# Performance work log

Measured on AMD Instinct MI355X. Metric: run time of the kernel, lower is better.

The kernel has to match this reference:

```python
import jax, jax.numpy as jnp
import numpy as np

NUM_USERS = 100000
NUM_ITEMS = 50000
EMBED_DIM = 64
N_LAYERS = 3
NUM_EDGES = 3276800  # avg user degree 32
BATCH = 16384


def setup_inputs() -> dict:
    key = jax.random.key(0)
    k0, k1, k2, k3, k4, k5 = jax.random.split(key, 6)
    rows = jax.random.randint(k0, (NUM_EDGES,), 0, NUM_USERS, dtype=jnp.int32)
    cols = jax.random.randint(k1, (NUM_EDGES,), 0, NUM_ITEMS, dtype=jnp.int32)
    user_table = jax.random.normal(k2, (NUM_USERS, EMBED_DIM), dtype=jnp.float32) * 0.1
    item_table = jax.random.normal(k3, (NUM_ITEMS, EMBED_DIM), dtype=jnp.float32) * 0.1
    user_indices = jax.random.randint(k4, (BATCH,), 0, NUM_USERS, dtype=jnp.int32)
    item_indices = jax.random.randint(k5, (BATCH,), 0, NUM_ITEMS, dtype=jnp.int32)
    return {
        "user_table": user_table,
        "item_table": item_table,
        "rows": rows,
        "cols": cols,
        "user_indices": user_indices,
        "item_indices": item_indices,
    }


def reference(user_table, item_table, rows, cols, user_indices, item_indices):
    # D^-1 A row-normalization of the binary bipartite adjacency:
    # normalized edge value for edge (u, i) is 1 / deg(u) (0 if isolated).
    ones = jnp.ones(rows.shape, dtype=user_table.dtype)
    deg = jax.ops.segment_sum(ones, rows, num_segments=NUM_USERS)
    inv_deg = jnp.where(deg > 0, 1.0 / deg, 0.0)
    vals = inv_deg[rows]  # [E]

    u = user_table  # [U, D] (unused by propagation in the original too)
    it = item_table  # [I, D]
    for _ in range(N_LAYERS):
        # u = A @ it  (SpMM via gather + segment-sum over destination users)
        u = jax.ops.segment_sum(vals[:, None] * it[cols], rows, num_segments=NUM_USERS)
        # it = A^T @ u
        it = jax.ops.segment_sum(vals[:, None] * u[rows], cols, num_segments=NUM_ITEMS)

    scores = jnp.sum(u[user_indices] * it[item_indices], axis=-1)  # [B]
    return jax.nn.sigmoid(scores)
```

## Files before the change

### kernel.cpp

```cpp
#include <hip/hip_runtime.h>
#include <math.h>

#define NUM_USERS 100000
#define NUM_ITEMS 50000
#define EMBED     64
#define NUM_EDGES 3276800
#define BATCH     16384
#define CAP       12800
#define NBUCK     391
#define P1_EDGES  8192
#define P1_THREADS 512
#define P2_THREADS 1024
#define CVT_GROUPS (NUM_ITEMS * 8)
#define CVT_BLOCKS ((CVT_GROUPS + P1_THREADS - 1) / P1_THREADS)

typedef _Float16 half8 __attribute__((ext_vector_type(8)));

__global__ void __launch_bounds__(P1_THREADS)
build_kernel(const int* __restrict__ rows, const int* __restrict__ cols,
             const float* __restrict__ itab, _Float16* __restrict__ it16,
             _Float16* __restrict__ w16,
             int* __restrict__ ucur, int* __restrict__ icur,
             int* __restrict__ rec_u, int* __restrict__ rec_i) {
    __shared__ int hu[400], hi[400], gu[400], gi[400];
    __shared__ int lbase[400], lcur[400];
    __shared__ int sc[512];
    __shared__ int recbuf[P1_EDGES];
    int t = threadIdx.x;

    if (blockIdx.x >= 400) {
        int b = blockIdx.x - 400;
        if (b < CVT_BLOCKS) {
            int i = b * P1_THREADS + t;
            if (i < CVT_GROUPS) {
                const float4* p = (const float4*)itab + 2 * i;
                float4 a = p[0], c = p[1];
                half8 o;
                o[0] = (_Float16)a.x; o[1] = (_Float16)a.y; o[2] = (_Float16)a.z; o[3] = (_Float16)a.w;
                o[4] = (_Float16)c.x; o[5] = (_Float16)c.y; o[6] = (_Float16)c.z; o[7] = (_Float16)c.w;
                ((half8*)it16)[i] = o;
            }
        } else {
            if (t < 64) w16[(long long)NUM_USERS * EMBED + t] = (_Float16)0.f;
            else if (t < 128) it16[(long long)NUM_ITEMS * EMBED + (t - 64)] = (_Float16)0.f;
        }
        return;
    }

    long long e0 = (long long)blockIdx.x * P1_EDGES;
    int er[16], ec[16];
    #pragma unroll
    for (int q = 0; q < 16; ++q) {
        er[q] = rows[e0 + t + q * P1_THREADS];
        ec[q] = cols[e0 + t + q * P1_THREADS];
    }

    for (int i = t; i < 400; i += P1_THREADS) { hu[i] = 0; hi[i] = 0; }
    __syncthreads();
    #pragma unroll
    for (int q = 0; q < 16; ++q) {
        atomicAdd(&hu[er[q] >> 8], 1);
        atomicAdd(&hi[ec[q] >> 7], 1);
    }
    __syncthreads();
    for (int i = t; i < 400; i += P1_THREADS) {
        int vr = (hu[i] + 15) & ~15;
        gu[i] = vr ? atomicAdd(&ucur[i], vr) : 0;
        vr = (hi[i] + 15) & ~15;
        gi[i] = vr ? atomicAdd(&icur[i], vr) : 0;
    }

    __syncthreads();
    sc[t] = (t < 400) ? hu[t] : 0;
    __syncthreads();
    for (int o = 1; o < 512; o <<= 1) {
        int x = (t >= o) ? sc[t - o] : 0; __syncthreads();
        sc[t] += x; __syncthreads();
    }
    if (t < 400) { lbase[t] = sc[t] - hu[t]; lcur[t] = 0; }
    __syncthreads();
    #pragma unroll
    for (int q = 0; q < 16; ++q) {
        int b = er[q] >> 8;
        int p = lbase[b] + atomicAdd(&lcur[b], 1);
        recbuf[p] = (ec[q] << 8) | (er[q] & 255);
    }
    __syncthreads();
    sc[t] = (t < 400) ? ((hu[t] + 15) & ~15) : 0;
    __syncthreads();
    for (int o = 1; o < 512; o <<= 1) {
        int x = (t >= o) ? sc[t - o] : 0; __syncthreads();
        sc[t] += x; __syncthreads();
    }
    int total = sc[511];
    for (int o4 = t * 4; o4 < total; o4 += P1_THREADS * 4) {
        int lo = 0, hi_ = 399;
        while (lo < hi_) { int mid = (lo + hi_) >> 1; if (sc[mid] > o4) hi_ = mid; else lo = mid + 1; }
        int b = lo;
        int v = hu[b];
        int vr = (v + 15) & ~15;
        int j = o4 - (sc[b] - vr);
        int gpos = gu[b] + j;
        if (gpos + 3 < CAP) {
            int4 val;
            val.x = (j + 0 < v) ? recbuf[lbase[b] + j + 0] : -1;
            val.y = (j + 1 < v) ? recbuf[lbase[b] + j + 1] : -1;
            val.z = (j + 2 < v) ? recbuf[lbase[b] + j + 2] : -1;
            val.w = (j + 3 < v) ? recbuf[lbase[b] + j + 3] : -1;
            *(int4*)(rec_u + (long long)b * CAP + gpos) = val;
        } else {
            for (int k = 0; k < 4; ++k)
                if (gpos + k < CAP)
                    rec_u[(long long)b * CAP + gpos + k] = (j + k < v) ? recbuf[lbase[b] + j + k] : -1;
        }
    }

    __syncthreads();
    sc[t] = (t < 400) ? hi[t] : 0;
    __syncthreads();
    for (int o = 1; o < 512; o <<= 1) {
        int x = (t >= o) ? sc[t - o] : 0; __syncthreads();
        sc[t] += x; __syncthreads();
    }
    if (t < 400) { lbase[t] = sc[t] - hi[t]; lcur[t] = 0; }
    __syncthreads();
    #pragma unroll
    for (int q = 0; q < 16; ++q) {
        int b = ec[q] >> 7;
        int p = lbase[b] + atomicAdd(&lcur[b], 1);
        recbuf[p] = (er[q] << 7) | (ec[q] & 127);
    }
    __syncthreads();
    sc[t] = (t < 400) ? ((hi[t] + 15) & ~15) : 0;
    __syncthreads();
    for (int o = 1; o < 512; o <<= 1) {
        int x = (t >= o) ? sc[t - o] : 0; __syncthreads();
        sc[t] += x; __syncthreads();
    }
    total = sc[511];
    for (int o4 = t * 4; o4 < total; o4 += P1_THREADS * 4) {
        int lo = 0, hi_ = 399;
        while (lo < hi_) { int mid = (lo + hi_) >> 1; if (sc[mid] > o4) hi_ = mid; else lo = mid + 1; }
        int b = lo;
        int v = hi[b];
        int vr = (v + 15) & ~15;
        int j = o4 - (sc[b] - vr);
        int gpos = gi[b] + j;
        if (gpos + 3 < CAP) {
            int4 val;
            val.x = (j + 0 < v) ? recbuf[lbase[b] + j + 0] : -1;
            val.y = (j + 1 < v) ? recbuf[lbase[b] + j + 1] : -1;
            val.z = (j + 2 < v) ? recbuf[lbase[b] + j + 2] : -1;
            val.w = (j + 3 < v) ? recbuf[lbase[b] + j + 3] : -1;
            *(int4*)(rec_i + (long long)b * CAP + gpos) = val;
        } else {
            for (int k = 0; k < 4; ++k)
                if (gpos + k < CAP)
                    rec_i[(long long)b * CAP + gpos + k] = (j + k < v) ? recbuf[lbase[b] + j + k] : -1;
        }
    }
}

template <int VBITS>
__device__ __forceinline__ void pass2_body(int* __restrict__ rec, const int* __restrict__ cur,
                                           int* __restrict__ deg, int* __restrict__ off,
                                           float* __restrict__ inv32, int ncap, int b,
                                           int* buf, int* h, int* ex, int* cnt, int* sc) {
    const int V = 1 << VBITS, M = V - 1;
    int t = threadIdx.x;
    long long s = (long long)b * CAP;
    int n = cur[b]; if (n > CAP) n = CAP;
    int nv = (n + 3) >> 2;
    const int4* rec4 = (const int4*)(rec + s);
    for (int i = t; i < nv; i += P2_THREADS) {
        int4 v4 = rec4[i];
        buf[4 * i + 0] = v4.x; buf[4 * i + 1] = v4.y;
        buf[4 * i + 2] = v4.z; buf[4 * i + 3] = v4.w;
    }
    if (t < V) { h[t] = 0; cnt[t] = 0; }
    __syncthreads();
    for (int i = t; i < n; i += P2_THREADS) {
        int r = buf[i];
        if (r != -1) atomicAdd(&h[r & M], 1);
    }
    __syncthreads();
    if (t < V) sc[t] = h[t];
    __syncthreads();
    for (int o = 1; o < V; o <<= 1) {
        int x = (t >= o && t < V) ? sc[t - o] : 0;
        __syncthreads();
        if (t < V) sc[t] += x;
        __syncthreads();
    }
    if (t < V) {
        ex[t] = sc[t] - h[t];
        int id = b * V + t;
        if (id < ncap) {
            int v = h[t];
            deg[id] = v;
            off[id] = (int)(s + ex[t]);
            if (inv32) inv32[id] = v ? 1.0f / (float)v : 0.0f;
        }
    }
    __syncthreads();
    for (int i = t; i < n; i += P2_THREADS) {
        int r = buf[i];
        if (r == -1) continue;
        int k = r & M;
        int rnk = atomicAdd(&cnt[k], 1);
        rec[s + ex[k] + rnk] = (int)(((unsigned)r) >> VBITS);
    }
}

__global__ void __launch_bounds__(P2_THREADS)
pass2_kernel(int* __restrict__ rec_u, const int* __restrict__ ucur,
             int* __restrict__ udeg, int* __restrict__ uoff, float* __restrict__ inv32,
             int* __restrict__ rec_i, const int* __restrict__ icur,
             int* __restrict__ ideg, int* __restrict__ ioff) {
    __shared__ int buf[CAP];
    __shared__ int h[256], ex[256], cnt[256], sc[256];
    if (blockIdx.x < NBUCK)
        pass2_body<8>(rec_u, ucur, udeg, uoff, inv32, NUM_USERS, blockIdx.x,
                      buf, h, ex, cnt, sc);
    else
        pass2_body<7>(rec_i, icur, ideg, ioff, (float*)nullptr, NUM_ITEMS,
                      blockIdx.x - NBUCK, buf, h, ex, cnt, sc);
}

__global__ void gather_u(const int* __restrict__ uoff, const int* __restrict__ udeg,
                         const int* __restrict__ csr_col, const float* __restrict__ inv32,
                         const _Float16* __restrict__ it, _Float16* __restrict__ w) {
    int row = blockIdx.x * 4 + (threadIdx.x >> 6);
    if (row >= NUM_USERS) return;
    int lane = threadIdx.x & 63;
    int slot = lane >> 3;
    int h    = lane & 7;
    int start = uoff[row];
    int end = start + udeg[row];
    half8 acc = {0, 0, 0, 0, 0, 0, 0, 0};
    for (int k = start; k < end; k += 64) {
        int e1 = end - 1;
        int idx[8], c[8];
        #pragma unroll
        for (int q = 0; q < 8; ++q) {
            idx[q] = k + slot + q * 8;
            int safe = idx[q] < e1 ? idx[q] : e1;
            c[q] = csr_col[safe];
            c[q] = idx[q] < end ? c[q] : NUM_ITEMS;
        }
        half8 x[8];
        #pragma unroll
        for (int q = 0; q < 8; ++q)
            x[q] = *(const half8*)(it + (long long)c[q] * EMBED + (h << 3));
        #pragma unroll
        for (int q = 0; q < 8; ++q) acc += x[q];
    }
    float f[8];
    #pragma unroll
    for (int j = 0; j < 8; ++j) {
        f[j] = (float)acc[j];
        f[j] += __shfl_xor(f[j], 8, 64);
        f[j] += __shfl_xor(f[j], 16, 64);
        f[j] += __shfl_xor(f[j], 32, 64);
    }
    if (lane < 8) {
        float v = inv32[row];
        float v2 = v * v;
        half8 ow;
        #pragma unroll
        for (int j = 0; j < 8; ++j) ow[j] = (_Float16)(f[j] * v2);
        *(half8*)(w + (long long)row * EMBED + (lane << 3)) = ow;
    }
}

__global__ void gather_it(const int* __restrict__ ioff, const int* __restrict__ ideg,
                          const int* __restrict__ csc_row,
                          const _Float16* __restrict__ w, _Float16* __restrict__ it) {
    int col = blockIdx.x * 4 + (threadIdx.x >> 6);
    if (col >= NUM_ITEMS) return;
    int lane = threadIdx.x & 63;
    int slot = lane >> 3;
    int h    = lane & 7;
    int start = ioff[col];
    int end = start + ideg[col];
    half8 acc = {0, 0, 0, 0, 0, 0, 0, 0};
    for (int k = start; k < end; k += 64) {
        int e1 = end - 1;
        int idx[8], r[8];
        #pragma unroll
        for (int q = 0; q < 8; ++q) {
            idx[q] = k + slot + q * 8;
            int safe = idx[q] < e1 ? idx[q] : e1;
            r[q] = csc_row[safe];
            r[q] = idx[q] < end ? r[q] : NUM_USERS;
        }
        half8 x[8];
        #pragma unroll
        for (int q = 0; q < 8; ++q)
            x[q] = *(const half8*)(w + (long long)r[q] * EMBED + (h << 3));
        #pragma unroll
        for (int q = 0; q < 8; ++q) acc += x[q];
    }
    float f[8];
    #pragma unroll
    for (int j = 0; j < 8; ++j) {
        f[j] = (float)acc[j];
        f[j] += __shfl_xor(f[j], 8, 64);
        f[j] += __shfl_xor(f[j], 16, 64);
        f[j] += __shfl_xor(f[j], 32, 64);
    }
    if (lane < 8) {
        half8 o;
        #pragma unroll
        for (int j = 0; j < 8; ++j) o[j] = (_Float16)f[j];
        *(half8*)(it + (long long)col * EMBED + (lane << 3)) = o;
    }
}

__global__ void batch_score(const int* __restrict__ ioff, const int* __restrict__ ideg,
                            const int* __restrict__ csc_row, const _Float16* __restrict__ w,
                            const int* __restrict__ udeg,
                            const int* __restrict__ uidx, const int* __restrict__ iidx,
                            float* __restrict__ out) {
    int b = blockIdx.x * 4 + (threadIdx.x >> 6);
    if (b >= BATCH) return;
    int lane = threadIdx.x & 63;
    int col = iidx[b];
    int slot = lane >> 3;
    int h    = lane & 7;
    int start = ioff[col];
    int end = start + ideg[col];
    half8 acc = {0, 0, 0, 0, 0, 0, 0, 0};
    for (int k = start; k < end; k += 64) {
        int e1 = end - 1;
        int idx[8], r[8];
        #pragma unroll
        for (int q = 0; q < 8; ++q) {
            idx[q] = k + slot + q * 8;
            int safe = idx[q] < e1 ? idx[q] : e1;
            r[q] = csc_row[safe];
            r[q] = idx[q] < end ? r[q] : NUM_USERS;
        }
        half8 x[8];
        #pragma unroll
        for (int q = 0; q < 8; ++q)
            x[q] = *(const half8*)(w + (long long)r[q] * EMBED + (h << 3));
        #pragma unroll
        for (int q = 0; q < 8; ++q) acc += x[q];
    }
    float f[8];
    #pragma unroll
    for (int j = 0; j < 8; ++j) {
        f[j] = (float)acc[j];
        f[j] += __shfl_xor(f[j], 8, 64);
        f[j] += __shfl_xor(f[j], 16, 64);
        f[j] += __shfl_xor(f[j], 32, 64);
    }
    int ui = uidx[b];
    half8 wv = *(const half8*)(w + (long long)ui * EMBED + (h << 3));
    float p = 0.f;
    #pragma unroll
    for (int j = 0; j < 8; ++j) p += f[j] * (float)wv[j];
    p += __shfl_xor(p, 1, 64);
    p += __shfl_xor(p, 2, 64);
    p += __shfl_xor(p, 4, 64);
    if (lane == 0) {
        float s = p * (float)udeg[ui];
        out[b] = 1.0f / (1.0f + expf(-s));
    }
}

extern "C" void kernel_launch(void* const* d_in, const int* in_sizes, int n_in,
                              void* d_out, int out_size, void* d_ws, size_t ws_size,
                              hipStream_t stream) {
    const float* item_table = (const float*)d_in[1];
    const int*   rows       = (const int*)d_in[2];
    const int*   cols       = (const int*)d_in[3];
    const int*   uidx       = (const int*)d_in[4];
    const int*   iidx       = (const int*)d_in[5];
    float* out = (float*)d_out;

    char* base = (char*)d_ws;
    int*   udeg  = (int*)(base + 0);
    int*   ideg  = (int*)(base +   400000);
    int*   uoff  = (int*)(base +   600000);
    int*   ioff  = (int*)(base +  1000000);
    float* inv32 = (float*)(base + 1200000);
    int*   ucur  = (int*)(base +  1600000);
    int*   icur  = (int*)(base +  1601600);
    int*   rec_u = (int*)(base +  1720320);
    int*   rec_i = (int*)(base + 22200320);
    _Float16* w16  = (_Float16*)(base + 42680320);
    _Float16* it16 = (_Float16*)(base + 55480448);

    (void)hipMemsetAsync(ucur, 0, 3200, stream);

    build_kernel<<<400 + CVT_BLOCKS + 1, P1_THREADS, 0, stream>>>(
        rows, cols, item_table, it16, w16, ucur, icur, rec_u, rec_i);
    pass2_kernel<<<NBUCK * 2, P2_THREADS, 0, stream>>>(rec_u, ucur, udeg, uoff, inv32,
                                                       rec_i, icur, ideg, ioff);

    const int ublocks = (NUM_USERS + 3) / 4;
    const int iblocks = (NUM_ITEMS + 3) / 4;
    for (int l = 0; l < 3; ++l) {
        gather_u<<<ublocks, 256, 0, stream>>>(uoff, udeg, rec_u, inv32, it16, w16);
        if (l < 2)
            gather_it<<<iblocks, 256, 0, stream>>>(ioff, ideg, rec_i, w16, it16);
    }
    batch_score<<<BATCH / 4, 256, 0, stream>>>(ioff, ideg, rec_i, w16, udeg,
                                               uidx, iidx, out);
}
```

Before: 411.4 us.

## Pad CSR segments to 16 and store byte offsets for vectorized gather

Each per-row adjacency segment is padded to a multiple of 16 with sentinel entries that point at a zero row, and the stored indices are pre-scaled to byte offsets. The gather kernels can then read indices as int4/int2 vectors with no bounds clamping or per-element masking. The slot reduction now shuffles packed fp16 pairs instead of eight separate floats. In exchange, padding may overflow CAP in dense buckets, the sentinel writes are serial per thread, and reducing in fp16 loses some precision.

```diff
diff --git a/kernel.cpp b/kernel.cpp
--- a/kernel.cpp
+++ b/kernel.cpp
@@ -15,6 +15,23 @@
 #define CVT_BLOCKS ((CVT_GROUPS + P1_THREADS - 1) / P1_THREADS)
 
 typedef _Float16 half8 __attribute__((ext_vector_type(8)));
+
+union H8 { half8 v; int i[4]; };
+
+__device__ __forceinline__ half8 slot_reduce(half8 acc) {
+    H8 a; a.v = acc;
+    H8 o;
+    #pragma unroll
+    for (int j = 0; j < 4; ++j) o.i[j] = __shfl_xor(a.i[j], 8, 64);
+    a.v += o.v;
+    #pragma unroll
+    for (int j = 0; j < 4; ++j) o.i[j] = __shfl_xor(a.i[j], 16, 64);
+    a.v += o.v;
+    #pragma unroll
+    for (int j = 0; j < 4; ++j) o.i[j] = __shfl_xor(a.i[j], 32, 64);
+    a.v += o.v;
+    return a.v;
+}
 
 __global__ void __launch_bounds__(P1_THREADS)
 build_kernel(const int* __restrict__ rows, const int* __restrict__ cols,
@@ -164,7 +181,7 @@
 template <int VBITS>
 __device__ __forceinline__ void pass2_body(int* __restrict__ rec, const int* __restrict__ cur,
                                            int* __restrict__ deg, int* __restrict__ off,
-                                           float* __restrict__ inv32, int ncap, int b,
+                                           float* __restrict__ inv32, int ncap, int b, int sentinel,
                                            int* buf, int* h, int* ex, int* cnt, int* sc) {
     const int V = 1 << VBITS, M = V - 1;
     int t = threadIdx.x;
@@ -184,7 +201,7 @@
         if (r != -1) atomicAdd(&h[r & M], 1);
     }
     __syncthreads();
-    if (t < V) sc[t] = h[t];
+    if (t < V) sc[t] = (h[t] + 15) & ~15;
     __syncthreads();
     for (int o = 1; o < V; o <<= 1) {
         int x = (t >= o && t < V) ? sc[t - o] : 0;
@@ -193,14 +210,17 @@
         __syncthreads();
     }
     if (t < V) {
-        ex[t] = sc[t] - h[t];
+        int ph = (h[t] + 15) & ~15;
+        int pb = sc[t] - ph;
+        ex[t] = pb;
         int id = b * V + t;
         if (id < ncap) {
             int v = h[t];
             deg[id] = v;
-            off[id] = (int)(s + ex[t]);
+            off[id] = (int)(s + pb);
             if (inv32) inv32[id] = v ? 1.0f / (float)v : 0.0f;
         }
+        for (int j = h[t]; j < ph && pb + j < CAP; ++j) rec[s + pb + j] = sentinel;
     }
     __syncthreads();
     for (int i = t; i < n; i += P2_THREADS) {
@@ -208,7 +228,9 @@
         if (r == -1) continue;
         int k = r & M;
         int rnk = atomicAdd(&cnt[k], 1);
-        rec[s + ex[k] + rnk] = (int)(((unsigned)r) >> VBITS);
+        int p = ex[k] + rnk;
+        if (p < CAP)
+            rec[s + p] = (int)((((unsigned)r) >> VBITS) << 7);
     }
 }
 
@@ -221,14 +243,14 @@
     __shared__ int h[256], ex[256], cnt[256], sc[256];
     if (blockIdx.x < NBUCK)
         pass2_body<8>(rec_u, ucur, udeg, uoff, inv32, NUM_USERS, blockIdx.x,
-                      buf, h, ex, cnt, sc);
+                      NUM_ITEMS << 7, buf, h, ex, cnt, sc);
     else
         pass2_body<7>(rec_i, icur, ideg, ioff, (float*)nullptr, NUM_ITEMS,
-                      blockIdx.x - NBUCK, buf, h, ex, cnt, sc);
+                      blockIdx.x - NBUCK, NUM_USERS << 7, buf, h, ex, cnt, sc);
 }
 
 __global__ void gather_u(const int* __restrict__ uoff, const int* __restrict__ udeg,
-                         const int* __restrict__ csr_col, const float* __restrict__ inv32,
+                         const int* __restrict__ csr_boff, const float* __restrict__ inv32,
                          const _Float16* __restrict__ it, _Float16* __restrict__ w) {
     int row = blockIdx.x * 4 + (threadIdx.x >> 6);
     if (row >= NUM_USERS) return;
@@ -236,45 +258,38 @@
     int slot = lane >> 3;
     int h    = lane & 7;
     int start = uoff[row];
-    int end = start + udeg[row];
-    half8 acc = {0, 0, 0, 0, 0, 0, 0, 0};
-    for (int k = start; k < end; k += 64) {
-        int e1 = end - 1;
-        int idx[8], c[8];
-        #pragma unroll
-        for (int q = 0; q < 8; ++q) {
-            idx[q] = k + slot + q * 8;
-            int safe = idx[q] < e1 ? idx[q] : e1;
-            c[q] = csr_col[safe];
-            c[q] = idx[q] < end ? c[q] : NUM_ITEMS;
-        }
-        half8 x[8];
-        #pragma unroll
-        for (int q = 0; q < 8; ++q)
-            x[q] = *(const half8*)(it + (long long)c[q] * EMBED + (h << 3));
-        #pragma unroll
-        for (int q = 0; q < 8; ++q) acc += x[q];
-    }
-    float f[8];
-    #pragma unroll
-    for (int j = 0; j < 8; ++j) {
-        f[j] = (float)acc[j];
-        f[j] += __shfl_xor(f[j], 8, 64);
-        f[j] += __shfl_xor(f[j], 16, 64);
-        f[j] += __shfl_xor(f[j], 32, 64);
-    }
+    int pend = start + ((udeg[row] + 15) & ~15);
+    const char* itb = (const char*)it;
+    unsigned hoff = (unsigned)(h << 4);
+    half8 acc = {};
+    int k = start;
+    for (; k + 32 <= pend; k += 32) {
+        int4 o4 = *(const int4*)(csr_boff + k + slot * 4);
+        half8 x0 = *(const half8*)(itb + ((unsigned)o4.x + hoff));
+        half8 x1 = *(const half8*)(itb + ((unsigned)o4.y + hoff));
+        half8 x2 = *(const half8*)(itb + ((unsigned)o4.z + hoff));
+        half8 x3 = *(const half8*)(itb + ((unsigned)o4.w + hoff));
+        acc += (x0 + x1) + (x2 + x3);
+    }
+    if (k < pend) {
+        int2 o2 = *(const int2*)(csr_boff + k + slot * 2);
+        half8 x0 = *(const half8*)(itb + ((unsigned)o2.x + hoff));
+        half8 x1 = *(const half8*)(itb + ((unsigned)o2.y + hoff));
+        acc += x0 + x1;
+    }
+    half8 r = slot_reduce(acc);
     if (lane < 8) {
         float v = inv32[row];
         float v2 = v * v;
         half8 ow;
         #pragma unroll
-        for (int j = 0; j < 8; ++j) ow[j] = (_Float16)(f[j] * v2);
+        for (int j = 0; j < 8; ++j) ow[j] = (_Float16)((float)r[j] * v2);
         *(half8*)(w + (long long)row * EMBED + (lane << 3)) = ow;
     }
 }
 
 __global__ void gather_it(const int* __restrict__ ioff, const int* __restrict__ ideg,
-                          const int* __restrict__ csc_row,
+                          const int* __restrict__ csc_boff,
                           const _Float16* __restrict__ w, _Float16* __restrict__ it) {
     int col = blockIdx.x * 4 + (threadIdx.x >> 6);
     if (col >= NUM_ITEMS) return;
@@ -282,43 +297,32 @@
     int slot = lane >> 3;
     int h    = lane & 7;
     int start = ioff[col];
-    int end = start + ideg[col];
-    half8 acc = {0, 0, 0, 0, 0, 0, 0, 0};
-    for (int k = start; k < end; k += 64) {
-        int e1 = end - 1;
-        int idx[8], r[8];
-        #pragma unroll
-        for (int q = 0; q < 8; ++q) {
-            idx[q] = k + slot + q * 8;
-            int safe = idx[q] < e1 ? idx[q] : e1;
-            r[q] = csc_row[safe];
-            r[q] = idx[q] < end ? r[q] : NUM_USERS;
-        }
-        half8 x[8];
-        #pragma unroll
-        for (int q = 0; q < 8; ++q)
-            x[q] = *(const half8*)(w + (long long)r[q] * EMBED + (h << 3));
-        #pragma unroll
-        for (int q = 0; q < 8; ++q) acc += x[q];
-    }
-    float f[8];
-    #pragma unroll
-    for (int j = 0; j < 8; ++j) {
-        f[j] = (float)acc[j];
-        f[j] += __shfl_xor(f[j], 8, 64);
-        f[j] += __shfl_xor(f[j], 16, 64);
-        f[j] += __shfl_xor(f[j], 32, 64);
-    }
-    if (lane < 8) {
-        half8 o;
-        #pragma unroll
-        for (int j = 0; j < 8; ++j) o[j] = (_Float16)f[j];
-        *(half8*)(it + (long long)col * EMBED + (lane << 3)) = o;
-    }
+    int pend = start + ((ideg[col] + 15) & ~15);
+    const char* wb = (const char*)w;
+    unsigned hoff = (unsigned)(h << 4);
+    half8 acc = {};
+    int k = start;
+    for (; k + 32 <= pend; k += 32) {
+        int4 o4 = *(const int4*)(csc_boff + k + slot * 4);
+        half8 x0 = *(const half8*)(wb + ((unsigned)o4.x + hoff));
+        half8 x1 = *(const half8*)(wb + ((unsigned)o4.y + hoff));
+        half8 x2 = *(const half8*)(wb + ((unsigned)o4.z + hoff));
+        half8 x3 = *(const half8*)(wb + ((unsigned)o4.w + hoff));
+        acc += (x0 + x1) + (x2 + x3);
+    }
+    if (k < pend) {
+        int2 o2 = *(const int2*)(csc_boff + k + slot * 2);
+        half8 x0 = *(const half8*)(wb + ((unsigned)o2.x + hoff));
+        half8 x1 = *(const half8*)(wb + ((unsigned)o2.y + hoff));
+        acc += x0 + x1;
+    }
+    half8 r = slot_reduce(acc);
+    if (lane < 8)
+        *(half8*)(it + (long long)col * EMBED + (lane << 3)) = r;
 }
 
 __global__ void batch_score(const int* __restrict__ ioff, const int* __restrict__ ideg,
-                            const int* __restrict__ csc_row, const _Float16* __restrict__ w,
+                            const int* __restrict__ csc_boff, const _Float16* __restrict__ w,
                             const int* __restrict__ udeg,
                             const int* __restrict__ uidx, const int* __restrict__ iidx,
                             float* __restrict__ out) {
@@ -329,38 +333,31 @@
     int slot = lane >> 3;
     int h    = lane & 7;
     int start = ioff[col];
-    int end = start + ideg[col];
-    half8 acc = {0, 0, 0, 0, 0, 0, 0, 0};
-    for (int k = start; k < end; k += 64) {
-        int e1 = end - 1;
-        int idx[8], r[8];
-        #pragma unroll
-        for (int q = 0; q < 8; ++q) {
-            idx[q] = k + slot + q * 8;
-            int safe = idx[q] < e1 ? idx[q] : e1;
-            r[q] = csc_row[safe];
-            r[q] = idx[q] < end ? r[q] : NUM_USERS;
-        }
-        half8 x[8];
-        #pragma unroll
-        for (int q = 0; q < 8; ++q)
-            x[q] = *(const half8*)(w + (long long)r[q] * EMBED + (h << 3));
-        #pragma unroll
-        for (int q = 0; q < 8; ++q) acc += x[q];
-    }
-    float f[8];
-    #pragma unroll
-    for (int j = 0; j < 8; ++j) {
-        f[j] = (float)acc[j];
-        f[j] += __shfl_xor(f[j], 8, 64);
-        f[j] += __shfl_xor(f[j], 16, 64);
-        f[j] += __shfl_xor(f[j], 32, 64);
-    }
+    int pend = start + ((ideg[col] + 15) & ~15);
+    const char* wb = (const char*)w;
+    unsigned hoff = (unsigned)(h << 4);
+    half8 acc = {};
+    int k = start;
+    for (; k + 32 <= pend; k += 32) {
+        int4 o4 = *(const int4*)(csc_boff + k + slot * 4);
+        half8 x0 = *(const half8*)(wb + ((unsigned)o4.x + hoff));
+        half8 x1 = *(const half8*)(wb + ((unsigned)o4.y + hoff));
+        half8 x2 = *(const half8*)(wb + ((unsigned)o4.z + hoff));
+        half8 x3 = *(const half8*)(wb + ((unsigned)o4.w + hoff));
+        acc += (x0 + x1) + (x2 + x3);
+    }
+    if (k < pend) {
+        int2 o2 = *(const int2*)(csc_boff + k + slot * 2);
+        half8 x0 = *(const half8*)(wb + ((unsigned)o2.x + hoff));
+        half8 x1 = *(const half8*)(wb + ((unsigned)o2.y + hoff));
+        acc += x0 + x1;
+    }
+    half8 r = slot_reduce(acc);
     int ui = uidx[b];
     half8 wv = *(const half8*)(w + (long long)ui * EMBED + (h << 3));
     float p = 0.f;
     #pragma unroll
-    for (int j = 0; j < 8; ++j) p += f[j] * (float)wv[j];
+    for (int j = 0; j < 8; ++j) p += (float)r[j] * (float)wv[j];
     p += __shfl_xor(p, 1, 64);
     p += __shfl_xor(p, 2, 64);
     p += __shfl_xor(p, 4, 64);
```

Result: faster. 403.2 us (-2.0%).
